# Optimization experiments

Measured on AMD Instinct MI355X. Metric: run time of the kernel, lower is better.

The kernel has to match this reference:

```python
import jax, jax.numpy as jnp
import numpy as np

D_MODEL = 1024
NUM_HEADS = 16


def setup_inputs() -> dict:
    key = jax.random.key(0)
    ks = jax.random.split(key, 5)
    scale = 1.0 / np.sqrt(D_MODEL)
    X = jax.random.normal(ks[0], (4, 2048, D_MODEL), dtype=jnp.float32)
    W_q = jax.random.normal(ks[1], (D_MODEL, D_MODEL), dtype=jnp.float32) * scale
    W_k = jax.random.normal(ks[2], (D_MODEL, D_MODEL), dtype=jnp.float32) * scale
    W_v = jax.random.normal(ks[3], (D_MODEL, D_MODEL), dtype=jnp.float32) * scale
    W_o = jax.random.normal(ks[4], (D_MODEL, D_MODEL), dtype=jnp.float32) * scale
    return {"X": X, "W_q": W_q, "W_k": W_k, "W_v": W_v, "W_o": W_o}


def reference(X, W_q, W_k, W_v, W_o):
    b, s, d_model = X.shape
    h = NUM_HEADS
    d_k = d_model // h
    # Linear projections (y = x @ W^T convention; W stored as [out,in] would be
    # x @ W.T, but with random weights we use x @ W — math is identical in form).
    def split_heads(y):
        return y.reshape(b, s, h, d_k).transpose(0, 2, 1, 3)  # b h s d
    q = split_heads(X @ W_q)
    k = split_heads(X @ W_k)
    v = split_heads(X @ W_v)
    scores = jnp.einsum('bhid,bhjd->bhij', q, k) / jnp.sqrt(jnp.float32(d_k))
    causal = jnp.tril(jnp.ones((s, s), dtype=bool))
    scores = jnp.where(causal[None, None], scores, jnp.float32(-jnp.inf))
    probs = jax.nn.softmax(scores, axis=-1)
    attended = jnp.einsum('bhij,bhjd->bhid', probs, v)
    out = attended.transpose(0, 2, 1, 3).reshape(b, s, d_model)
    return out @ W_o
```

## Files before the change

### kernel.cpp

```cpp
#include <hip/hip_runtime.h>

typedef __bf16 bf16;
typedef __attribute__((ext_vector_type(8))) __bf16 bf16x8;
typedef __attribute__((ext_vector_type(4))) float f32x4;
typedef __attribute__((ext_vector_type(16))) float f32x16;
typedef __attribute__((ext_vector_type(4))) unsigned short u16x4;
typedef __attribute__((ext_vector_type(2))) int v2i;

#define D_MODEL 1024
#define SEQ     2048
#define NB      4
#define NH      16
#define DK      64
#define MROWS   (NB * SEQ)

#define MFMA_BF16 __builtin_amdgcn_mfma_f32_16x16x32_bf16
#define MFMA32    __builtin_amdgcn_mfma_f32_32x32x16_bf16
#define EXP2F(x) __builtin_amdgcn_exp2f(x)
#define QSCALE 0.18033688011112042f

__device__ __forceinline__ bf16 f2b(float f) {
    union { float f; unsigned u; } c; c.f = f;
    unsigned r = (c.u + 0x7fffu + ((c.u >> 16) & 1u)) >> 16;
    union { unsigned short s; bf16 b; } o; o.s = (unsigned short)r;
    return o.b;
}
__device__ __forceinline__ unsigned short f2u(float f) {
    union { float f; unsigned u; } c; c.f = f;
    return (unsigned short)((c.u + 0x7fffu + ((c.u >> 16) & 1u)) >> 16);
}

__device__ __forceinline__ f32x16 zero16() {
    f32x16 z = {0.f,0.f,0.f,0.f,0.f,0.f,0.f,0.f,
                0.f,0.f,0.f,0.f,0.f,0.f,0.f,0.f};
    return z;
}

template <int N> struct IC { static constexpr int v = N; };

__global__ void prep_kernel(const float* __restrict__ X,
                            const float* __restrict__ Wq, const float* __restrict__ Wk,
                            const float* __restrict__ Wv, const float* __restrict__ Wo,
                            bf16* __restrict__ Xb, bf16* __restrict__ WqkvT,
                            bf16* __restrict__ WoT) {
    __shared__ float tile[32][33];
    const int bid = blockIdx.x;
    if (bid < 8192) {
        int i = bid * 256 + threadIdx.x;
        float4 v = ((const float4*)X)[i];
        u16x4 o; o[0] = f2u(v.x); o[1] = f2u(v.y); o[2] = f2u(v.z); o[3] = f2u(v.w);
        ((u16x4*)Xb)[i] = o;
    } else {
        int r = bid - 8192;
        int w = r >> 10, tl = r & 1023;
        const float* src = (w == 0) ? Wq : (w == 1) ? Wk : (w == 2) ? Wv : Wo;
        bf16* dst = (w == 3) ? WoT : WqkvT + (size_t)w * 1024 * 1024;
        const int n0 = (tl & 31) * 32, k0 = (tl >> 5) * 32;
        const int tx = threadIdx.x & 31, ty = threadIdx.x >> 5;
#pragma unroll
        for (int i = 0; i < 4; i++)
            tile[ty + i * 8][tx] = src[(size_t)(k0 + ty + i * 8) * 1024 + n0 + tx];
        __syncthreads();
#pragma unroll
        for (int i = 0; i < 4; i++)
            dst[(size_t)(n0 + ty + i * 8) * 1024 + k0 + tx] = f2b(tile[tx][ty + i * 8]);
    }
}

__global__ __launch_bounds__(256) void gemm_qkv(const bf16* __restrict__ A,
                                                const bf16* __restrict__ Bt,
                                                bf16* __restrict__ outQ,
                                                bf16* __restrict__ outV) {
    __shared__ __align__(16) bf16 lA[128 * 64];
    __shared__ __align__(16) bf16 lB[128 * 64];

    const int t = threadIdx.x;
    const int wid = t >> 6, lane = t & 63;
    const int ln = lane & 15, qd = lane >> 4;
    const int wm = wid >> 1, wn = wid & 1;

    const int bid = blockIdx.x;
    const int idx = bid >> 3;
    const int colb = (bid & 7) * 3 + (idx % 3);
    const int rowb = idx / 3;
    const int row0 = rowb * 128, col0 = colb * 128;
    const bool isQK = (col0 < 2048);

    const int srow = t >> 3;
    const int schunk = (t & 7) ^ (srow & 7);
    const bf16* ga = A  + (size_t)(row0 + srow) * 1024 + schunk * 8;
    const bf16* gb = Bt + (size_t)(col0 + srow) * 1024 + schunk * 8;
    const int swk = ln & 7;

    f32x4 acc[4][4];
#pragma unroll
    for (int i = 0; i < 4; i++)
#pragma unroll
        for (int j = 0; j < 4; j++) acc[i][j] = (f32x4){0.f, 0.f, 0.f, 0.f};

    for (int kb = 0; kb < 1024; kb += 64) {
#pragma unroll
        for (int c = 0; c < 4; c++) {
            __builtin_amdgcn_global_load_lds(
                (const __attribute__((address_space(1))) void*)(ga + kb + (size_t)c * 32 * 1024),
                (__attribute__((address_space(3))) void*)(&lA[t * 8 + c * 2048]), 16, 0, 0);
            __builtin_amdgcn_global_load_lds(
                (const __attribute__((address_space(1))) void*)(gb + kb + (size_t)c * 32 * 1024),
                (__attribute__((address_space(3))) void*)(&lB[t * 8 + c * 2048]), 16, 0, 0);
        }
        __syncthreads();

#pragma unroll
        for (int ks = 0; ks < 2; ks++) {
            bf16x8 af[4], bfr[4];
#pragma unroll
            for (int i = 0; i < 4; i++)
                af[i] = *(const bf16x8*)&lA[(wm * 64 + i * 16 + ln) * 64
                                            + ((ks * 4 + qd) ^ swk) * 8];
#pragma unroll
            for (int j = 0; j < 4; j++)
                bfr[j] = *(const bf16x8*)&lB[(wn * 64 + j * 16 + ln) * 64
                                             + ((ks * 4 + qd) ^ swk) * 8];
            if (isQK) {
#pragma unroll
                for (int i = 0; i < 4; i++)
#pragma unroll
                    for (int j = 0; j < 4; j++)
                        acc[i][j] = MFMA_BF16(bfr[j], af[i], acc[i][j], 0, 0, 0);
            } else {
#pragma unroll
                for (int i = 0; i < 4; i++)
#pragma unroll
                    for (int j = 0; j < 4; j++)
                        acc[i][j] = MFMA_BF16(af[i], bfr[j], acc[i][j], 0, 0, 0);
            }
        }
        __syncthreads();
    }

    if (isQK) {
#pragma unroll
        for (int i = 0; i < 4; i++)
#pragma unroll
            for (int j = 0; j < 4; j++) {
                int m  = row0 + wm * 64 + i * 16 + ln;
                int n0 = col0 + wn * 64 + j * 16 + qd * 4;
                float scale = (n0 < 1024) ? QSCALE : 1.0f;
                int b = m >> 11, s = m & 2047;
                int h = (n0 & 1023) >> 6, d0 = n0 & 63;
                size_t addr = (((size_t)(b * NH + h) * SEQ + s) * DK + d0)
                              + (size_t)(n0 >> 10) * 8388608;
                u16x4 w;
#pragma unroll
                for (int r = 0; r < 4; r++) w[r] = f2u(acc[i][j][r] * scale);
                *(u16x4*)&outQ[addr] = w;
            }
    } else {
#pragma unroll
        for (int i = 0; i < 4; i++)
#pragma unroll
            for (int j = 0; j < 4; j++) {
                int m0 = row0 + wm * 64 + i * 16 + qd * 4;
                int n  = col0 + wn * 64 + j * 16 + ln - 2048;
                int b = m0 >> 11, s0 = m0 & 2047;
                int h = n >> 6, d = n & 63;
                size_t addr = ((size_t)(b * NH + h) * DK + d) * SEQ + s0;
                u16x4 w;
#pragma unroll
                for (int r = 0; r < 4; r++) w[r] = f2u(acc[i][j][r]);
                *(u16x4*)&outV[addr] = w;
            }
    }
}

__global__ __launch_bounds__(256) void gemm_o(const bf16* __restrict__ A,
                                              const bf16* __restrict__ Bt,
                                              float* __restrict__ out) {
    __shared__ __align__(16) bf16 lA[128 * 64];
    __shared__ __align__(16) bf16 lB[128 * 64];

    const int t = threadIdx.x;
    const int wid = t >> 6, lane = t & 63;
    const int ln = lane & 15, qd = lane >> 4;
    const int wm = wid >> 1, wn = wid & 1;

    const int bid = blockIdx.x;
    const int colb = bid & 7, rowb = bid >> 3;
    const int row0 = rowb * 128, col0 = colb * 128;

    const int srow = t >> 3;
    const int schunk = (t & 7) ^ (srow & 7);
    const bf16* ga = A  + (size_t)(row0 + srow) * 1024 + schunk * 8;
    const bf16* gb = Bt + (size_t)(col0 + srow) * 1024 + schunk * 8;
    const int swk = ln & 7;

    f32x4 acc[4][4];
#pragma unroll
    for (int i = 0; i < 4; i++)
#pragma unroll
        for (int j = 0; j < 4; j++) acc[i][j] = (f32x4){0.f, 0.f, 0.f, 0.f};

    for (int kb = 0; kb < 1024; kb += 64) {
#pragma unroll
        for (int c = 0; c < 4; c++) {
            __builtin_amdgcn_global_load_lds(
                (const __attribute__((address_space(1))) void*)(ga + kb + (size_t)c * 32 * 1024),
                (__attribute__((address_space(3))) void*)(&lA[t * 8 + c * 2048]), 16, 0, 0);
            __builtin_amdgcn_global_load_lds(
                (const __attribute__((address_space(1))) void*)(gb + kb + (size_t)c * 32 * 1024),
                (__attribute__((address_space(3))) void*)(&lB[t * 8 + c * 2048]), 16, 0, 0);
        }
        __syncthreads();

#pragma unroll
        for (int ks = 0; ks < 2; ks++) {
            bf16x8 af[4], bfr[4];
#pragma unroll
            for (int i = 0; i < 4; i++)
                af[i] = *(const bf16x8*)&lA[(wm * 64 + i * 16 + ln) * 64
                                            + ((ks * 4 + qd) ^ swk) * 8];
#pragma unroll
            for (int j = 0; j < 4; j++)
                bfr[j] = *(const bf16x8*)&lB[(wn * 64 + j * 16 + ln) * 64
                                             + ((ks * 4 + qd) ^ swk) * 8];
#pragma unroll
            for (int i = 0; i < 4; i++)
#pragma unroll
                for (int j = 0; j < 4; j++)
                    acc[i][j] = MFMA_BF16(bfr[j], af[i], acc[i][j], 0, 0, 0);
        }
        __syncthreads();
    }

#pragma unroll
    for (int i = 0; i < 4; i++)
#pragma unroll
        for (int j = 0; j < 4; j++) {
            int m  = row0 + wm * 64 + i * 16 + ln;
            int n0 = col0 + wn * 64 + j * 16 + qd * 4;
            *(f32x4*)&out[(size_t)m * 1024 + n0] = acc[i][j];
        }
}

__global__ __launch_bounds__(128, 2) void attn_kernel(const bf16* __restrict__ Q,
                                                      const bf16* __restrict__ K,
                                                      const bf16* __restrict__ Vt,
                                                      bf16* __restrict__ attn_out) {
    __shared__ __align__(16) bf16 smem[4][64 * 64];

    const int t = threadIdx.x;
    const int wid = t >> 6, lane = t & 63;
    const int qcol = lane & 31, h = lane >> 5;

    const int bid = blockIdx.x;
    const int bh = ((bid >> 7) << 3) | (bid & 7);
    const int p  = (bid >> 3) & 15;
    const int gA = 31 - p, gB = p;
    const int ntA = gA + 1;

    const bf16* Qh = Q  + (size_t)bh * SEQ * DK;
    const bf16* Kh = K  + (size_t)bh * SEQ * DK;
    const bf16* Vh = Vt + (size_t)bh * DK * SEQ;

    const int srow = t >> 3;
    const int schunk = (t & 7) ^ (srow & 7);
    const bf16* kgp = Kh + (size_t)srow * DK + schunk * 8;
    const bf16* vgp = Vh + (size_t)srow * SEQ + schunk * 8;

    const char* sbase = (const char*)&smem[0][0];
    int raddr[4];
#pragma unroll
    for (int tt = 0; tt < 4; tt++)
        raddr[tt] = qcol * 128 + (((2 * tt + h) ^ (lane & 7)) * 16);

    int qw0;
    bf16x8 qf[4];
    f32x16 o[2];
    float l;

    auto initGroup = [&](int g) {
        qw0 = g * 64 + wid * 32;
#pragma unroll
        for (int tt = 0; tt < 4; tt++)
            qf[tt] = *(const bf16x8*)(Qh + (size_t)(qw0 + qcol) * DK + tt * 16 + h * 8);
        o[0] = zero16(); o[1] = zero16();
        l = 0.f;
    };

    const int b = bh >> 4, head = bh & 15;
    auto finalize = [&]() {
        float ll = l + __shfl_xor(l, 32);
        const float inv = 1.0f / ll;
        const size_t orow = ((size_t)(b * SEQ + qw0 + qcol)) * D_MODEL + head * DK;
#pragma unroll
        for (int m = 0; m < 2; m++)
#pragma unroll
            for (int q4 = 0; q4 < 4; q4++) {
                u16x4 w;
#pragma unroll
                for (int c = 0; c < 4; c++) w[c] = f2u(o[m][q4 * 4 + c] * inv);
                *(u16x4*)&attn_out[orow + m * 32 + q4 * 8 + h * 4] = w;
            }
    };

    auto stage = [&](int kb, int buf) {
#pragma unroll
        for (int c = 0; c < 4; c++) {
            __builtin_amdgcn_global_load_lds(
                (const __attribute__((address_space(1))) void*)(kgp + (size_t)(kb + c * 16) * DK),
                (__attribute__((address_space(3))) void*)(&smem[buf][t * 8 + c * 1024]), 16, 0, 0);
            __builtin_amdgcn_global_load_lds(
                (const __attribute__((address_space(1))) void*)(vgp + (size_t)c * 16 * SEQ + kb),
                (__attribute__((address_space(3))) void*)(&smem[2 + buf][t * 8 + c * 1024]), 16, 0, 0);
        }
    };

    auto qkt = [&](const char* kb_base) -> f32x16 {
        f32x16 z = zero16();
#pragma unroll
        for (int tt = 0; tt < 4; tt++) {
            bf16x8 kf = *(const bf16x8*)(kb_base + raddr[tt]);
            z = MFMA32(kf, qf[tt], z, 0, 0, 0);
        }
        return z;
    };

    auto pvks = [&](const f32x16& s, int b8, int ks, const char* vbase) {
        unsigned A, B, C, D;
        asm("v_cvt_pk_bf16_f32 %0, %1, %2"
            : "=v"(A) : "v"(s[b8 + 0]), "v"(s[b8 + 1]));
        asm("v_cvt_pk_bf16_f32 %0, %1, %2"
            : "=v"(B) : "v"(s[b8 + 2]), "v"(s[b8 + 3]));
        asm("v_cvt_pk_bf16_f32 %0, %1, %2"
            : "=v"(C) : "v"(s[b8 + 4]), "v"(s[b8 + 5]));
        asm("v_cvt_pk_bf16_f32 %0, %1, %2"
            : "=v"(D) : "v"(s[b8 + 6]), "v"(s[b8 + 7]));
        v2i r02 = __builtin_amdgcn_permlane32_swap((int)A, (int)C, false, false);
        v2i r13 = __builtin_amdgcn_permlane32_swap((int)B, (int)D, false, false);
        union { unsigned u[4]; bf16x8 v; } pf;
        pf.u[0] = (unsigned)r02[0];
        pf.u[1] = (unsigned)r13[0];
        pf.u[2] = (unsigned)r02[1];
        pf.u[3] = (unsigned)r13[1];
#pragma unroll
        for (int m = 0; m < 2; m++) {
            bf16x8 vf = *(const bf16x8*)(vbase + raddr[ks] + m * 4096);
            o[m] = MFMA32(vf, pf.v, o[m], 0, 0, 0);
        }
    };

    auto smaxFull = [&](f32x16& s) -> float {
#pragma unroll
        for (int r = 0; r < 16; r++) s[r] = EXP2F(s[r]);
        float s0 = (s[0] + s[1]) + (s[2] + s[3]);
        float s1 = (s[4] + s[5]) + (s[6] + s[7]);
        float s2 = (s[8] + s[9]) + (s[10] + s[11]);
        float s3 = (s[12] + s[13]) + (s[14] + s[15]);
        return (s0 + s1) + (s2 + s3);
    };

    auto compute = [&](auto curc, int kb) {
        constexpr int CUR = decltype(curc)::v;
        const char* kbase = sbase + CUR * 8192;
        const char* vbase = sbase + 16384 + CUR * 8192;
        const int rel = qw0 - kb;
        if (rel < 0) return;
        if (rel >= 64) {
            __builtin_amdgcn_s_setprio(1);
            f32x16 s0 = qkt(kbase);
            f32x16 s1 = qkt(kbase + 4096);
            __builtin_amdgcn_s_setprio(0);
            l += smaxFull(s0);
            __builtin_amdgcn_s_setprio(1);
            pvks(s0, 0, 0, vbase);
            pvks(s0, 8, 1, vbase);
            __builtin_amdgcn_s_setprio(0);
            l += smaxFull(s1);
            __builtin_amdgcn_s_setprio(1);
            pvks(s1, 0, 2, vbase);
            pvks(s1, 8, 3, vbase);
            __builtin_amdgcn_s_setprio(0);
        } else {
            const int nt = (rel >> 5) + 1;
            f32x16 st[2];
#pragma unroll
            for (int n = 0; n < 2; n++)
                if (n < nt) st[n] = qkt(kbase + n * 4096);
            float ps = 0.f;
#pragma unroll
            for (int n = 0; n < 2; n++)
                if (n < nt) {
                    const bool diag = (rel == 32 * n);
#pragma unroll
                    for (int r = 0; r < 16; r++) {
                        float pv = EXP2F(st[n][r]);
                        if (diag) {
                            const int kloc = (r & 3) + 8 * (r >> 2) + 4 * h;
                            pv = (kloc > qcol) ? 0.f : pv;
                        }
                        st[n][r] = pv;
                    }
                    float s0 = (st[n][0] + st[n][1]) + (st[n][2] + st[n][3]);
                    float s1 = (st[n][4] + st[n][5]) + (st[n][6] + st[n][7]);
                    float s2 = (st[n][8] + st[n][9]) + (st[n][10] + st[n][11]);
                    float s3 = (st[n][12] + st[n][13]) + (st[n][14] + st[n][15]);
                    ps += (s0 + s1) + (s2 + s3);
                }
            l += ps;
#pragma unroll
            for (int ks = 0; ks < 4; ks++)
                if (ks < 2 * nt)
                    pvks(st[ks >> 1], (ks & 1) * 8, ks, vbase);
        }
    };

    auto step = [&](auto curc, int i) {
        constexpr int CUR = decltype(curc)::v;
        __syncthreads();
        const int nx = i + 1;
        if (nx < 33) {
            const int tnx = (nx < ntA) ? nx : nx - ntA;
            stage(tnx * 64, CUR ^ 1);
        }
        const int kb = ((i < ntA) ? i : i - ntA) * 64;
        compute(curc, kb);
        if (i == ntA - 1) { finalize(); initGroup(gB); }
    };

    stage(0, 0);
    initGroup(gA);

    step(IC<0>{}, 0);
#pragma unroll 1
    for (int ii = 0; ii < 16; ii++) {
        step(IC<1>{}, 2 * ii + 1);
        step(IC<0>{}, 2 * ii + 2);
    }
    finalize();
}

extern "C" void kernel_launch(void* const* d_in, const int* in_sizes, int n_in,
                              void* d_out, int out_size, void* d_ws, size_t ws_size,
                              hipStream_t stream) {
    const float* X  = (const float*)d_in[0];
    const float* Wq = (const float*)d_in[1];
    const float* Wk = (const float*)d_in[2];
    const float* Wv = (const float*)d_in[3];
    const float* Wo = (const float*)d_in[4];
    float* out = (float*)d_out;
    char* ws = (char*)d_ws;

    bf16* Xb    = (bf16*)(ws);
    bf16* WqkvT = (bf16*)(ws + (16u << 20));
    bf16* WoT   = (bf16*)(ws + (22u << 20));
    bf16* Qb    = (bf16*)(ws + (24u << 20));
    bf16* Vt    = (bf16*)(ws + (56u << 20));
    bf16* Attn  = Xb;
    bf16* Kb    = Qb + (size_t)8388608;

    prep_kernel<<<dim3(12288), dim3(256), 0, stream>>>(X, Wq, Wk, Wv, Wo,
                                                       Xb, WqkvT, WoT);

    gemm_qkv<<<dim3(1536), dim3(256), 0, stream>>>(Xb, WqkvT, Qb, Vt);

    attn_kernel<<<dim3(1024), dim3(128), 0, stream>>>(Qb, Kb, Vt, Attn);

    gemm_o<<<dim3(512), dim3(256), 0, stream>>>(Attn, WoT, out);
}
```

Measured before the change: 240.5 us.

## Rewrite QKV GEMM with 256x256 tiles and double-buffered LDS pipeline

The QKV projection GEMM moves from 128x128 tiles with 256 threads and single-buffered LDS to 256x256 tiles with 512 threads (8 waves). It double-buffers LDS (128KB) and prefetches the next K-tile's A and B halves in stages between MFMA quadrants. Explicit waitcnt and barriers control the schedule, and setprio raises priority during MFMA bursts. The goal is more data reuse per tile and hiding global load latency behind compute. The cost is far fewer workgroups (384), a large LDS footprint that limits occupancy, and a fragile hand-built synchronization schedule.

After: 344.8 us. 43.4% more time.

```diff
diff --git a/kernel.cpp b/kernel.cpp
--- a/kernel.cpp
+++ b/kernel.cpp
@@ -18,6 +18,10 @@
 #define MFMA32    __builtin_amdgcn_mfma_f32_32x32x16_bf16
 #define EXP2F(x) __builtin_amdgcn_exp2f(x)
 #define QSCALE 0.18033688011112042f
+
+#define BARRIER() do { asm volatile("" ::: "memory"); \
+                       __builtin_amdgcn_s_barrier();  \
+                       asm volatile("" ::: "memory"); } while (0)
 
 __device__ __forceinline__ bf16 f2b(float f) {
     union { float f; unsigned u; } c; c.f = f;
@@ -67,83 +71,161 @@
     }
 }
 
-__global__ __launch_bounds__(256) void gemm_qkv(const bf16* __restrict__ A,
-                                                const bf16* __restrict__ Bt,
-                                                bf16* __restrict__ outQ,
-                                                bf16* __restrict__ outV) {
-    __shared__ __align__(16) bf16 lA[128 * 64];
-    __shared__ __align__(16) bf16 lB[128 * 64];
+__global__ __launch_bounds__(512, 2) void gemm_qkv(const bf16* __restrict__ A,
+                                                   const bf16* __restrict__ Bt,
+                                                   bf16* __restrict__ outQ,
+                                                   bf16* __restrict__ outV) {
+    __shared__ __align__(16) char lds[131072];
 
     const int t = threadIdx.x;
     const int wid = t >> 6, lane = t & 63;
     const int ln = lane & 15, qd = lane >> 4;
-    const int wm = wid >> 1, wn = wid & 1;
-
-    const int bid = blockIdx.x;
-    const int idx = bid >> 3;
-    const int colb = (bid & 7) * 3 + (idx % 3);
-    const int rowb = idx / 3;
-    const int row0 = rowb * 128, col0 = colb * 128;
+    const int wm = wid >> 2, wn = wid & 3;
+    const int swk = ln & 7;
+
+    const int wg = (blockIdx.x & 7) * 48 + (blockIdx.x >> 3);
+    const int rowb = wg & 31, colb = wg >> 5;
+    const int row0 = rowb * 256, col0 = colb * 256;
     const bool isQK = (col0 < 2048);
 
     const int srow = t >> 3;
     const int schunk = (t & 7) ^ (srow & 7);
     const bf16* ga = A  + (size_t)(row0 + srow) * 1024 + schunk * 8;
     const bf16* gb = Bt + (size_t)(col0 + srow) * 1024 + schunk * 8;
-    const int swk = ln & 7;
-
-    f32x4 acc[4][4];
-#pragma unroll
-    for (int i = 0; i < 4; i++)
+
+    auto stageA = [&](int kt, int hc, int buf) {
+#pragma unroll
+        for (int L = 0; L < 2; L++)
+            __builtin_amdgcn_global_load_lds(
+                (const __attribute__((address_space(1))) void*)
+                    (ga + (size_t)(hc * 128 + L * 64) * 1024 + kt * 64),
+                (__attribute__((address_space(3))) void*)
+                    (lds + buf * 65536 + hc * 16384 + L * 8192 + t * 16), 16, 0, 0);
+    };
+    auto stageB = [&](int kt, int hc, int buf) {
+#pragma unroll
+        for (int L = 0; L < 2; L++)
+            __builtin_amdgcn_global_load_lds(
+                (const __attribute__((address_space(1))) void*)
+                    (gb + (size_t)(hc * 128 + L * 64) * 1024 + kt * 64),
+                (__attribute__((address_space(3))) void*)
+                    (lds + buf * 65536 + 32768 + hc * 16384 + L * 8192 + t * 16), 16, 0, 0);
+    };
+
+    const char* pABase = lds + (wm * 128 + ln) * 128;
+    const char* pBBase = lds + 32768 + (wn * 64 + ln) * 128;
+    const int cks0 = (qd ^ swk) * 16;
+    const int cks1 = ((4 + qd) ^ swk) * 16;
+
+    f32x4 acc[8][4];
+#pragma unroll
+    for (int i = 0; i < 8; i++)
 #pragma unroll
         for (int j = 0; j < 4; j++) acc[i][j] = (f32x4){0.f, 0.f, 0.f, 0.f};
 
-    for (int kb = 0; kb < 1024; kb += 64) {
-#pragma unroll
-        for (int c = 0; c < 4; c++) {
-            __builtin_amdgcn_global_load_lds(
-                (const __attribute__((address_space(1))) void*)(ga + kb + (size_t)c * 32 * 1024),
-                (__attribute__((address_space(3))) void*)(&lA[t * 8 + c * 2048]), 16, 0, 0);
-            __builtin_amdgcn_global_load_lds(
-                (const __attribute__((address_space(1))) void*)(gb + kb + (size_t)c * 32 * 1024),
-                (__attribute__((address_space(3))) void*)(&lB[t * 8 + c * 2048]), 16, 0, 0);
-        }
-        __syncthreads();
-
-#pragma unroll
-        for (int ks = 0; ks < 2; ks++) {
-            bf16x8 af[4], bfr[4];
-#pragma unroll
-            for (int i = 0; i < 4; i++)
-                af[i] = *(const bf16x8*)&lA[(wm * 64 + i * 16 + ln) * 64
-                                            + ((ks * 4 + qd) ^ swk) * 8];
-#pragma unroll
-            for (int j = 0; j < 4; j++)
-                bfr[j] = *(const bf16x8*)&lB[(wn * 64 + j * 16 + ln) * 64
-                                             + ((ks * 4 + qd) ^ swk) * 8];
+    stageA(0, 0, 0); stageA(0, 1, 0);
+    stageB(0, 0, 0); stageB(0, 1, 0);
+    stageA(1, 0, 1); stageA(1, 1, 1);
+    asm volatile("s_waitcnt vmcnt(4)" ::: "memory");
+    BARRIER();
+
+    auto ktile = [&](auto bufc, int kt) {
+        constexpr int BUF = decltype(bufc)::v;
+        const char* pa0 = pABase + BUF * 65536 + cks0;
+        const char* pa1 = pABase + BUF * 65536 + cks1;
+        const char* pb0 = pBBase + BUF * 65536 + cks0;
+        const char* pb1 = pBBase + BUF * 65536 + cks1;
+
+        bf16x8 af[8][2], bfr[4][2];
+
+        auto quad = [&](int ih, int jh) {
+            __builtin_amdgcn_s_setprio(1);
             if (isQK) {
 #pragma unroll
-                for (int i = 0; i < 4; i++)
-#pragma unroll
-                    for (int j = 0; j < 4; j++)
-                        acc[i][j] = MFMA_BF16(bfr[j], af[i], acc[i][j], 0, 0, 0);
+                for (int i2 = 0; i2 < 4; i2++)
+#pragma unroll
+                    for (int j2 = 0; j2 < 2; j2++)
+#pragma unroll
+                        for (int ks = 0; ks < 2; ks++)
+                            acc[ih * 4 + i2][jh * 2 + j2] =
+                                MFMA_BF16(bfr[jh * 2 + j2][ks], af[ih * 4 + i2][ks],
+                                          acc[ih * 4 + i2][jh * 2 + j2], 0, 0, 0);
             } else {
 #pragma unroll
-                for (int i = 0; i < 4; i++)
-#pragma unroll
-                    for (int j = 0; j < 4; j++)
-                        acc[i][j] = MFMA_BF16(af[i], bfr[j], acc[i][j], 0, 0, 0);
+                for (int i2 = 0; i2 < 4; i2++)
+#pragma unroll
+                    for (int j2 = 0; j2 < 2; j2++)
+#pragma unroll
+                        for (int ks = 0; ks < 2; ks++)
+                            acc[ih * 4 + i2][jh * 2 + j2] =
+                                MFMA_BF16(af[ih * 4 + i2][ks], bfr[jh * 2 + j2][ks],
+                                          acc[ih * 4 + i2][jh * 2 + j2], 0, 0, 0);
             }
-        }
-        __syncthreads();
+            __builtin_amdgcn_s_setprio(0);
+        };
+
+#pragma unroll
+        for (int i = 0; i < 4; i++) {
+            af[i][0] = *(const bf16x8*)(pa0 + i * 2048);
+            af[i][1] = *(const bf16x8*)(pa1 + i * 2048);
+        }
+#pragma unroll
+        for (int j = 0; j < 2; j++) {
+            bfr[j][0] = *(const bf16x8*)(pb0 + j * 2048);
+            bfr[j][1] = *(const bf16x8*)(pb1 + j * 2048);
+        }
+        if (kt + 1 < 16) stageB(kt + 1, 0, BUF ^ 1);
+        asm volatile("s_waitcnt lgkmcnt(8)" ::: "memory");
+        BARRIER();
+        asm volatile("s_waitcnt lgkmcnt(0)" ::: "memory");
+        quad(0, 0);
+        BARRIER();
+
+#pragma unroll
+        for (int i = 0; i < 4; i++) {
+            af[4 + i][0] = *(const bf16x8*)(pa0 + (4 + i) * 2048);
+            af[4 + i][1] = *(const bf16x8*)(pa1 + (4 + i) * 2048);
+        }
+#pragma unroll
+        for (int j = 0; j < 2; j++) {
+            bfr[2 + j][0] = *(const bf16x8*)(pb0 + (2 + j) * 2048);
+            bfr[2 + j][1] = *(const bf16x8*)(pb1 + (2 + j) * 2048);
+        }
+        if (kt + 1 < 16) stageB(kt + 1, 1, BUF ^ 1);
+        asm volatile("s_waitcnt lgkmcnt(8)" ::: "memory");
+        BARRIER();
+        asm volatile("s_waitcnt lgkmcnt(0)" ::: "memory");
+        quad(1, 1);
+        BARRIER();
+
+        if (kt + 2 < 16) stageA(kt + 2, 0, BUF);
+        BARRIER();
+        quad(0, 1);
+        BARRIER();
+
+        if (kt + 2 < 16) stageA(kt + 2, 1, BUF);
+        BARRIER();
+        quad(1, 0);
+        if (kt + 2 < 16) {
+            asm volatile("s_waitcnt vmcnt(4)" ::: "memory");
+        } else if (kt + 1 < 16) {
+            asm volatile("s_waitcnt vmcnt(0)" ::: "memory");
+        }
+        BARRIER();
+    };
+
+#pragma unroll 1
+    for (int kt = 0; kt < 16; kt += 2) {
+        ktile(IC<0>{}, kt);
+        ktile(IC<1>{}, kt + 1);
     }
 
     if (isQK) {
 #pragma unroll
-        for (int i = 0; i < 4; i++)
+        for (int i = 0; i < 8; i++)
 #pragma unroll
             for (int j = 0; j < 4; j++) {
-                int m  = row0 + wm * 64 + i * 16 + ln;
+                int m  = row0 + wm * 128 + i * 16 + ln;
                 int n0 = col0 + wn * 64 + j * 16 + qd * 4;
                 float scale = (n0 < 1024) ? QSCALE : 1.0f;
                 int b = m >> 11, s = m & 2047;
@@ -157,10 +239,10 @@
             }
     } else {
 #pragma unroll
-        for (int i = 0; i < 4; i++)
+        for (int i = 0; i < 8; i++)
 #pragma unroll
             for (int j = 0; j < 4; j++) {
-                int m0 = row0 + wm * 64 + i * 16 + qd * 4;
+                int m0 = row0 + wm * 128 + i * 16 + qd * 4;
                 int n  = col0 + wn * 64 + j * 16 + ln - 2048;
                 int b = m0 >> 11, s0 = m0 & 2047;
                 int h = n >> 6, d = n & 63;
@@ -461,7 +543,7 @@
     prep_kernel<<<dim3(12288), dim3(256), 0, stream>>>(X, Wq, Wk, Wv, Wo,
                                                        Xb, WqkvT, WoT);
 
-    gemm_qkv<<<dim3(1536), dim3(256), 0, stream>>>(Xb, WqkvT, Qb, Vt);
+    gemm_qkv<<<dim3(384), dim3(512), 0, stream>>>(Xb, WqkvT, Qb, Vt);
 
     attn_kernel<<<dim3(1024), dim3(128), 0, stream>>>(Qb, Kb, Vt, Attn);
 
```

## Double-buffer QKV GEMM with async LDS prefetch and 256x128 tiles

Applied to the files above, without the earlier changes.

Restructures the QKV projection GEMM to use 512-thread blocks computing 256x128 tiles. Global-to-LDS loads are double-buffered so each k-tile's fetch overlaps the MFMA work of the previous tile, with explicit vmcnt waits and raw s_barrier in place of __syncthreads. It also raises MFMA wave priority and remaps block indices for L2 locality. The goal is to hide global load latency and halve barrier stalls per k-step, at the cost of 96KB LDS per block and tighter occupancy constraints.

New measurement: 253.0 us. 5.2% more time.

```diff
diff --git a/kernel.cpp b/kernel.cpp
--- a/kernel.cpp
+++ b/kernel.cpp
@@ -18,6 +18,10 @@
 #define MFMA32    __builtin_amdgcn_mfma_f32_32x32x16_bf16
 #define EXP2F(x) __builtin_amdgcn_exp2f(x)
 #define QSCALE 0.18033688011112042f
+
+#define BARRIER() do { asm volatile("" ::: "memory"); \
+                       __builtin_amdgcn_s_barrier();  \
+                       asm volatile("" ::: "memory"); } while (0)
 
 __device__ __forceinline__ bf16 f2b(float f) {
     union { float f; unsigned u; } c; c.f = f;
@@ -67,30 +71,51 @@
     }
 }
 
-__global__ __launch_bounds__(256) void gemm_qkv(const bf16* __restrict__ A,
-                                                const bf16* __restrict__ Bt,
-                                                bf16* __restrict__ outQ,
-                                                bf16* __restrict__ outV) {
-    __shared__ __align__(16) bf16 lA[128 * 64];
-    __shared__ __align__(16) bf16 lB[128 * 64];
+__global__ __launch_bounds__(512, 2) void gemm_qkv(const bf16* __restrict__ A,
+                                                   const bf16* __restrict__ Bt,
+                                                   bf16* __restrict__ outQ,
+                                                   bf16* __restrict__ outV) {
+    __shared__ __align__(16) char lds[98304];
 
     const int t = threadIdx.x;
     const int wid = t >> 6, lane = t & 63;
     const int ln = lane & 15, qd = lane >> 4;
     const int wm = wid >> 1, wn = wid & 1;
-
-    const int bid = blockIdx.x;
-    const int idx = bid >> 3;
-    const int colb = (bid & 7) * 3 + (idx % 3);
-    const int rowb = idx / 3;
-    const int row0 = rowb * 128, col0 = colb * 128;
+    const int swk = ln & 7;
+
+    const int wg = (blockIdx.x & 7) * 96 + (blockIdx.x >> 3);
+    const int rowb = wg & 31, colb = wg >> 5;
+    const int row0 = rowb * 256, col0 = colb * 128;
     const bool isQK = (col0 < 2048);
 
     const int srow = t >> 3;
     const int schunk = (t & 7) ^ (srow & 7);
     const bf16* ga = A  + (size_t)(row0 + srow) * 1024 + schunk * 8;
     const bf16* gb = Bt + (size_t)(col0 + srow) * 1024 + schunk * 8;
-    const int swk = ln & 7;
+
+    auto stageA = [&](int kt, int buf) {
+#pragma unroll
+        for (int c = 0; c < 4; c++)
+            __builtin_amdgcn_global_load_lds(
+                (const __attribute__((address_space(1))) void*)
+                    (ga + (size_t)(c * 64) * 1024 + kt * 64),
+                (__attribute__((address_space(3))) void*)
+                    (lds + buf * 32768 + c * 8192 + t * 16), 16, 0, 0);
+    };
+    auto stageB = [&](int kt, int buf) {
+#pragma unroll
+        for (int c = 0; c < 2; c++)
+            __builtin_amdgcn_global_load_lds(
+                (const __attribute__((address_space(1))) void*)
+                    (gb + (size_t)(c * 64) * 1024 + kt * 64),
+                (__attribute__((address_space(3))) void*)
+                    (lds + 65536 + buf * 16384 + c * 8192 + t * 16), 16, 0, 0);
+    };
+
+    const char* pABase = lds + (wm * 64 + ln) * 128;
+    const char* pBBase = lds + 65536 + (wn * 64 + ln) * 128;
+    const int cks0 = (qd ^ swk) * 16;
+    const int cks1 = ((4 + qd) ^ swk) * 16;
 
     f32x4 acc[4][4];
 #pragma unroll
@@ -98,44 +123,79 @@
 #pragma unroll
         for (int j = 0; j < 4; j++) acc[i][j] = (f32x4){0.f, 0.f, 0.f, 0.f};
 
-    for (int kb = 0; kb < 1024; kb += 64) {
-#pragma unroll
-        for (int c = 0; c < 4; c++) {
-            __builtin_amdgcn_global_load_lds(
-                (const __attribute__((address_space(1))) void*)(ga + kb + (size_t)c * 32 * 1024),
-                (__attribute__((address_space(3))) void*)(&lA[t * 8 + c * 2048]), 16, 0, 0);
-            __builtin_amdgcn_global_load_lds(
-                (const __attribute__((address_space(1))) void*)(gb + kb + (size_t)c * 32 * 1024),
-                (__attribute__((address_space(3))) void*)(&lB[t * 8 + c * 2048]), 16, 0, 0);
-        }
-        __syncthreads();
-
-#pragma unroll
-        for (int ks = 0; ks < 2; ks++) {
-            bf16x8 af[4], bfr[4];
+    stageA(0, 0); stageB(0, 0);
+    stageA(1, 1); stageB(1, 1);
+    asm volatile("s_waitcnt vmcnt(6)" ::: "memory");
+    BARRIER();
+
+    auto ktile = [&](auto bufc, int kt) {
+        constexpr int BUF = decltype(bufc)::v;
+        const char* pa0 = pABase + BUF * 32768 + cks0;
+        const char* pa1 = pABase + BUF * 32768 + cks1;
+        const char* pb0 = pBBase + BUF * 16384 + cks0;
+        const char* pb1 = pBBase + BUF * 16384 + cks1;
+
+        bf16x8 af[4][2], bfr[4][2];
+#pragma unroll
+        for (int i = 0; i < 4; i++) {
+            af[i][0] = *(const bf16x8*)(pa0 + i * 2048);
+            af[i][1] = *(const bf16x8*)(pa1 + i * 2048);
+        }
+#pragma unroll
+        for (int j = 0; j < 4; j++) {
+            bfr[j][0] = *(const bf16x8*)(pb0 + j * 2048);
+            bfr[j][1] = *(const bf16x8*)(pb1 + j * 2048);
+        }
+        asm volatile("s_waitcnt lgkmcnt(0)" ::: "memory");
+        __builtin_amdgcn_sched_barrier(0);
+        BARRIER();
+
+        __builtin_amdgcn_s_setprio(1);
+        if (isQK) {
 #pragma unroll
             for (int i = 0; i < 4; i++)
-                af[i] = *(const bf16x8*)&lA[(wm * 64 + i * 16 + ln) * 64
-                                            + ((ks * 4 + qd) ^ swk) * 8];
-#pragma unroll
-            for (int j = 0; j < 4; j++)
-                bfr[j] = *(const bf16x8*)&lB[(wn * 64 + j * 16 + ln) * 64
-                                             + ((ks * 4 + qd) ^ swk) * 8];
-            if (isQK) {
-#pragma unroll
-                for (int i = 0; i < 4; i++)
-#pragma unroll
-                    for (int j = 0; j < 4; j++)
-                        acc[i][j] = MFMA_BF16(bfr[j], af[i], acc[i][j], 0, 0, 0);
-            } else {
-#pragma unroll
-                for (int i = 0; i < 4; i++)
-#pragma unroll
-                    for (int j = 0; j < 4; j++)
-                        acc[i][j] = MFMA_BF16(af[i], bfr[j], acc[i][j], 0, 0, 0);
-            }
-        }
-        __syncthreads();
+#pragma unroll
+                for (int j = 0; j < 4; j++)
+                    acc[i][j] = MFMA_BF16(bfr[j][0], af[i][0], acc[i][j], 0, 0, 0);
+        } else {
+#pragma unroll
+            for (int i = 0; i < 4; i++)
+#pragma unroll
+                for (int j = 0; j < 4; j++)
+                    acc[i][j] = MFMA_BF16(af[i][0], bfr[j][0], acc[i][j], 0, 0, 0);
+        }
+        __builtin_amdgcn_s_setprio(0);
+
+        if (kt + 2 < 16) { stageA(kt + 2, BUF); stageB(kt + 2, BUF); }
+
+        __builtin_amdgcn_s_setprio(1);
+        if (isQK) {
+#pragma unroll
+            for (int i = 0; i < 4; i++)
+#pragma unroll
+                for (int j = 0; j < 4; j++)
+                    acc[i][j] = MFMA_BF16(bfr[j][1], af[i][1], acc[i][j], 0, 0, 0);
+        } else {
+#pragma unroll
+            for (int i = 0; i < 4; i++)
+#pragma unroll
+                for (int j = 0; j < 4; j++)
+                    acc[i][j] = MFMA_BF16(af[i][1], bfr[j][1], acc[i][j], 0, 0, 0);
+        }
+        __builtin_amdgcn_s_setprio(0);
+
+        if (kt + 2 < 16) {
+            asm volatile("s_waitcnt vmcnt(6)" ::: "memory");
+        } else if (kt + 1 < 16) {
+            asm volatile("s_waitcnt vmcnt(0)" ::: "memory");
+        }
+        BARRIER();
+    };
+
+#pragma unroll 1
+    for (int kt = 0; kt < 16; kt += 2) {
+        ktile(IC<0>{}, kt);
+        ktile(IC<1>{}, kt + 1);
     }
 
     if (isQK) {
@@ -461,7 +521,7 @@
     prep_kernel<<<dim3(12288), dim3(256), 0, stream>>>(X, Wq, Wk, Wv, Wo,
                                                        Xb, WqkvT, WoT);
 
-    gemm_qkv<<<dim3(1536), dim3(256), 0, stream>>>(Xb, WqkvT, Qb, Vt);
+    gemm_qkv<<<dim3(768), dim3(512), 0, stream>>>(Xb, WqkvT, Qb, Vt);
 
     attn_kernel<<<dim3(1024), dim3(128), 0, stream>>>(Qb, Kb, Vt, Attn);
 
```
